# Performance work log

Hardware: AMD Instinct MI355X
Metric: run time of the kernel (lower is better)

Reference implementation:

```python
import jax, jax.numpy as jnp
import numpy as np

B, S, E = 2, 2048, 2048
H, HD = 32, 64          # n_heads, head_dim
KV, REP = 8, 4          # n_kv_head, n_kv_head_rep (H == KV*REP)
NEG = -1e9


def setup_inputs() -> dict:
    key = jax.random.key(0)
    ks = jax.random.split(key, 6)
    x = jax.random.normal(ks[0], (B, S, E), dtype=jnp.float32)
    # Llama RoPE tables: angles[p, i] = p / 10000^(2i/HD)
    inv_freq = 1.0 / (10000.0 ** (jnp.arange(0, HD, 2, dtype=jnp.float32) / HD))
    angles = jnp.arange(S, dtype=jnp.float32)[:, None] * inv_freq[None, :]  # [S, HD/2]
    cos, sin = jnp.cos(angles), jnp.sin(angles)
    # causal additive mask [S, S]
    mask = jnp.where(jnp.tril(jnp.ones((S, S), dtype=bool)), 0.0, NEG).astype(jnp.float32)
    sc = 0.02
    wq = jax.random.normal(ks[1], (E, H * HD), dtype=jnp.float32) * sc
    wk = jax.random.normal(ks[2], (E, KV * HD), dtype=jnp.float32) * sc
    wv = jax.random.normal(ks[3], (E, KV * HD), dtype=jnp.float32) * sc
    wo = jax.random.normal(ks[4], (H * HD, E), dtype=jnp.float32) * sc
    return {"x": x, "cos": cos, "sin": sin, "mask": mask,
            "wq": wq, "wk": wk, "wv": wv, "wo": wo, "start_pos": 0}


def _rope(t, cos, sin):
    # t: [B, S, h, HD]; rotate consecutive pairs (Llama complex convention)
    tp = t.reshape(t.shape[:-1] + (HD // 2, 2))
    t1, t2 = tp[..., 0], tp[..., 1]
    c = cos[None, :, None, :]
    s = sin[None, :, None, :]
    out = jnp.stack([t1 * c - t2 * s, t1 * s + t2 * c], axis=-1)
    return out.reshape(t.shape)


def reference(x, cos, sin, mask, wq, wk, wv, wo, start_pos):
    b, s, _ = x.shape
    q = (x @ wq).reshape(b, s, H, HD)
    k = (x @ wk).reshape(b, s, KV, HD)
    v = (x @ wv).reshape(b, s, KV, HD)
    q = _rope(q, cos, sin)
    k = _rope(k, cos, sin)
    # KV-cache: with start_pos=0 and full-seq prefill, the cache slice
    # [:, :start_pos+s] is exactly the freshly written k/v, so use them directly.
    # Grouped attention without materializing repeated K/V:
    # q -> [b, KV, REP, s, HD]; k,v -> [b, KV, s, HD]
    qg = q.transpose(0, 2, 1, 3).reshape(b, KV, REP, s, HD)
    kg = k.transpose(0, 2, 1, 3)
    vg = v.transpose(0, 2, 1, 3)
    scale = 1.0 / jnp.sqrt(jnp.float32(HD))
    scores = jnp.einsum('bgrqd,bgkd->bgrqk', qg, kg) * scale + mask
    attn = jax.nn.softmax(scores, axis=-1)
    og = jnp.einsum('bgrqk,bgkd->bgrqd', attn, vg)     # [b, KV, REP, s, HD]
    out = og.reshape(b, H, s, HD).transpose(0, 2, 1, 3).reshape(b, s, H * HD)
    return out @ wo
```

## Files before the change

### kernel.cpp

```cpp
#include <hip/hip_runtime.h>
#include <stdint.h>

#define S_LEN 2048
#define NTOK  4096
#define EMB   2048
#define NHEAD 32
#define HDIM  64
#define NKVH  8

typedef __bf16 bf16x8 __attribute__((ext_vector_type(8)));
typedef float  f32x4  __attribute__((ext_vector_type(4)));

#define AS1 __attribute__((address_space(1)))
#define AS3 __attribute__((address_space(3)))

#if __has_builtin(__builtin_amdgcn_exp2f)
#define EXP2(x) __builtin_amdgcn_exp2f(x)
#else
#define EXP2(x) exp2f(x)
#endif

#define QSCALE 0.1803368867f

__device__ __forceinline__ uint16_t f2bf(float f) {
  uint32_t u = __float_as_uint(f);
  u += 0x7fffu + ((u >> 16) & 1u);
  return (uint16_t)(u >> 16);
}
__device__ __forceinline__ float bf2f(uint16_t h) {
  return __uint_as_float(((uint32_t)h) << 16);
}
__device__ __forceinline__ void gld16(const void* g, void* l) {
  __builtin_amdgcn_global_load_lds((const AS1 uint32_t*)g, (AS3 uint32_t*)l, 16, 0, 0);
}
__device__ __forceinline__ f32x4 mfma16(bf16x8 a, bf16x8 b, f32x4 c) {
  return __builtin_amdgcn_mfma_f32_16x16x32_bf16(a, b, c, 0, 0, 0);
}

__global__ void k_cvt(const float* __restrict__ in, uint16_t* __restrict__ out) {
  int i = (blockIdx.x * 256 + threadIdx.x) * 4;
  float4 v = *(const float4*)(in + i);
  ushort4 o;
  o.x = f2bf(v.x); o.y = f2bf(v.y); o.z = f2bf(v.z); o.w = f2bf(v.w);
  *(ushort4*)(out + i) = o;
}

__global__ void k_transpose(const float* __restrict__ in, uint16_t* __restrict__ out,
                            int R, int C) {
  __shared__ float tile[32][33];
  int c0 = blockIdx.x * 32, r0 = blockIdx.y * 32;
  int tx = threadIdx.x & 31, ty = threadIdx.x >> 5;
#pragma unroll
  for (int j = 0; j < 32; j += 8)
    tile[ty + j][tx] = in[(size_t)(r0 + ty + j) * C + c0 + tx];
  __syncthreads();
#pragma unroll
  for (int j = 0; j < 32; j += 8)
    out[(size_t)(c0 + ty + j) * R + r0 + tx] = f2bf(tile[tx][ty + j]);
}

__global__ void k_transpose_v(const uint16_t* __restrict__ qkv, uint16_t* __restrict__ out) {
  __shared__ uint16_t tile[32][33];
  int s0 = blockIdx.x * 32, hd0 = blockIdx.y * 32, bh = blockIdx.z;
  int b = bh >> 3, kvh = bh & 7;
  int tx = threadIdx.x & 31, ty = threadIdx.x >> 5;
#pragma unroll
  for (int j = 0; j < 32; j += 8)
    tile[ty + j][tx] =
        qkv[((size_t)b * S_LEN + s0 + ty + j) * 3072 + 2560 + kvh * 64 + hd0 + tx];
  __syncthreads();
#pragma unroll
  for (int j = 0; j < 32; j += 8)
    out[((size_t)bh * 64 + hd0 + ty + j) * S_LEN + s0 + tx] = tile[tx][ty + j];
}

template <int N_REP, typename OUT_T>
__global__ __launch_bounds__(512, 1) void k_gemm256(
    const uint16_t* __restrict__ A, const uint16_t* __restrict__ BT,
    OUT_T* __restrict__ C, int M, int N, int K) {
  constexpr int ROUNDS = 4 + N_REP;
  __shared__ uint16_t lds[2][16384 + N_REP * 4096];
  const int tid = threadIdx.x, lane = tid & 63, w = tid >> 6;
  const int wm = w >> 2, wn = w & 3;
  const int l16 = lane & 15, lg = lane >> 4;
  const int nbn = N / (N_REP * 64);
  const int nwg = gridDim.x, cpx = nwg >> 3;
  const int swz = ((int)blockIdx.x & 7) * cpx + ((int)blockIdx.x >> 3);
  const int bm = (swz / nbn) * 256, bn = (swz % nbn) * (N_REP * 64);

  f32x4 acc[8][N_REP] = {};

  const int srow = tid >> 3, sslot = tid & 7;
  const int schunk = (sslot ^ (srow & 7)) * 8;
  const uint16_t* Ag = A + (size_t)(bm + srow) * K + schunk;
  const uint16_t* Bg = BT + (size_t)(bn + srow) * K + schunk;

  auto stage = [&](int d, int r, int k0) {
    if (r < 4) gld16(Ag + (size_t)r * 64 * K + k0, &lds[d][r * 4096 + tid * 8]);
    else       gld16(Bg + (size_t)(r - 4) * 64 * K + k0, &lds[d][16384 + (r - 4) * 4096 + tid * 8]);
  };
  auto lda = [&](int d, int mf, int s) -> bf16x8 {
    int row = wm * 128 + mf * 16 + l16;
    int slot = (s * 4 + lg) ^ (row & 7);
    return *(const bf16x8*)(&lds[d][row * 64 + slot * 8]);
  };
  auto ldb = [&](int d, int nf, int s) -> bf16x8 {
    int row = wn * (N_REP * 16) + nf * 16 + l16;
    int slot = (s * 4 + lg) ^ (row & 7);
    return *(const bf16x8*)(&lds[d][16384 + row * 64 + slot * 8]);
  };

  const int NT = K >> 6;
#pragma unroll
  for (int r = 0; r < ROUNDS; ++r) stage(0, r, 0);
#pragma unroll
  for (int r = 0; r < 4; ++r) if (1 < NT) stage(1, r, 64);
  asm volatile("s_waitcnt vmcnt(4)" ::: "memory");
  __builtin_amdgcn_s_barrier();

  for (int kt = 0; kt < NT; ++kt) {
    const int cur = kt & 1;
    const int nk0 = (kt + 1) << 6, nnk0 = (kt + 2) << 6;
    const bool m1 = (kt + 1 < NT), m2 = (kt + 2 < NT);
    bf16x8 a[4][2], b0[N_REP / 2][2], b1[N_REP / 2][2];
#pragma unroll
    for (int mi = 0; mi < 4; ++mi) { a[mi][0] = lda(cur, mi, 0); a[mi][1] = lda(cur, mi, 1); }
#pragma unroll
    for (int ni = 0; ni < N_REP / 2; ++ni) { b0[ni][0] = ldb(cur, ni, 0); b0[ni][1] = ldb(cur, ni, 1); }
    __builtin_amdgcn_s_barrier();
    asm volatile("s_waitcnt lgkmcnt(0)" ::: "memory");
    __builtin_amdgcn_sched_barrier(0);
    __builtin_amdgcn_s_setprio(1);
#pragma unroll
    for (int mi = 0; mi < 4; ++mi)
#pragma unroll
      for (int ni = 0; ni < N_REP / 2; ++ni) {
        acc[mi][ni] = mfma16(a[mi][0], b0[ni][0], acc[mi][ni]);
        acc[mi][ni] = mfma16(a[mi][1], b0[ni][1], acc[mi][ni]);
      }
    __builtin_amdgcn_s_setprio(0);
    __builtin_amdgcn_s_barrier();
#pragma unroll
    for (int ni = 0; ni < N_REP / 2; ++ni) { b1[ni][0] = ldb(cur, N_REP / 2 + ni, 0); b1[ni][1] = ldb(cur, N_REP / 2 + ni, 1); }
    if (m1) {
#pragma unroll
      for (int r = 4; r < 4 + N_REP / 2; ++r) stage(cur ^ 1, r, nk0);
    }
    __builtin_amdgcn_s_barrier();
    asm volatile("s_waitcnt lgkmcnt(0)" ::: "memory");
    __builtin_amdgcn_sched_barrier(0);
    __builtin_amdgcn_s_setprio(1);
#pragma unroll
    for (int mi = 0; mi < 4; ++mi)
#pragma unroll
      for (int ni = 0; ni < N_REP / 2; ++ni) {
        acc[mi][N_REP / 2 + ni] = mfma16(a[mi][0], b1[ni][0], acc[mi][N_REP / 2 + ni]);
        acc[mi][N_REP / 2 + ni] = mfma16(a[mi][1], b1[ni][1], acc[mi][N_REP / 2 + ni]);
      }
    __builtin_amdgcn_s_setprio(0);
    __builtin_amdgcn_s_barrier();
#pragma unroll
    for (int mi = 0; mi < 4; ++mi) { a[mi][0] = lda(cur, 4 + mi, 0); a[mi][1] = lda(cur, 4 + mi, 1); }
    if (m1) {
#pragma unroll
      for (int r = 4 + N_REP / 2; r < ROUNDS; ++r) stage(cur ^ 1, r, nk0);
    }
    __builtin_amdgcn_s_barrier();
    asm volatile("s_waitcnt lgkmcnt(0)" ::: "memory");
    __builtin_amdgcn_sched_barrier(0);
    __builtin_amdgcn_s_setprio(1);
#pragma unroll
    for (int mi = 0; mi < 4; ++mi)
#pragma unroll
      for (int ni = 0; ni < N_REP / 2; ++ni) {
        acc[4 + mi][N_REP / 2 + ni] = mfma16(a[mi][0], b1[ni][0], acc[4 + mi][N_REP / 2 + ni]);
        acc[4 + mi][N_REP / 2 + ni] = mfma16(a[mi][1], b1[ni][1], acc[4 + mi][N_REP / 2 + ni]);
      }
    __builtin_amdgcn_s_setprio(0);
    __builtin_amdgcn_s_barrier();
    if (m2) {
#pragma unroll
      for (int r = 0; r < 4; ++r) stage(cur, r, nnk0);
    }
    __builtin_amdgcn_s_setprio(1);
#pragma unroll
    for (int mi = 0; mi < 4; ++mi)
#pragma unroll
      for (int ni = 0; ni < N_REP / 2; ++ni) {
        acc[4 + mi][ni] = mfma16(a[mi][0], b0[ni][0], acc[4 + mi][ni]);
        acc[4 + mi][ni] = mfma16(a[mi][1], b0[ni][1], acc[4 + mi][ni]);
      }
    __builtin_amdgcn_s_setprio(0);
    if (m2) { asm volatile("s_waitcnt vmcnt(4)" ::: "memory"); }
    else    { asm volatile("s_waitcnt vmcnt(0)" ::: "memory"); }
    __builtin_amdgcn_s_barrier();
  }
#pragma unroll
  for (int mf = 0; mf < 8; ++mf)
#pragma unroll
    for (int nf = 0; nf < N_REP; ++nf)
#pragma unroll
      for (int r = 0; r < 4; ++r) {
        int row = bm + wm * 128 + mf * 16 + lg * 4 + r;
        int col = bn + wn * (N_REP * 16) + nf * 16 + l16;
        float v = acc[mf][nf][r];
        if constexpr (sizeof(OUT_T) == 4) C[(size_t)row * N + col] = v;
        else                              C[(size_t)row * N + col] = f2bf(v);
      }
}

__global__ void k_rope(const uint16_t* __restrict__ qkv, const float* __restrict__ cosT,
                       const float* __restrict__ sinT, uint16_t* __restrict__ qb,
                       uint16_t* __restrict__ kb) {
  int idx = blockIdx.x * 256 + threadIdx.x;
  int row = idx / 1280;
  int col = (idx - row * 1280) * 2;
  int s = row & (S_LEN - 1);
  uint32_t vv = *(const uint32_t*)(qkv + (size_t)row * 3072 + col);
  float t1 = bf2f((uint16_t)vv), t2 = bf2f((uint16_t)(vv >> 16));
  int i = (col & 63) >> 1;
  if (col < 2048) {
    float c = cosT[s * 32 + i] * QSCALE, sn = sinT[s * 32 + i] * QSCALE;
    uint32_t o = (uint32_t)f2bf(t1 * c - t2 * sn) | ((uint32_t)f2bf(t1 * sn + t2 * c) << 16);
    *(uint32_t*)(qb + (size_t)row * 2048 + col) = o;
  } else {
    int cc = col - 2048;
    float c = cosT[s * 32 + i], sn = sinT[s * 32 + i];
    uint32_t o = (uint32_t)f2bf(t1 * c - t2 * sn) | ((uint32_t)f2bf(t1 * sn + t2 * c) << 16);
    *(uint32_t*)(kb + (size_t)row * 512 + cc) = o;
  }
}

template <bool MASKED>
__device__ __forceinline__ void tile_compute(
    const uint16_t* Kc, const uint16_t* Vc, const bf16x8 qf[2][2], bf16x8 onesv,
    int l16, int lg, int kv0, int qb0,
    float m_r[2], f32x4 lacc[2], f32x4 acc[2][4]) {
  f32x4 st[2][4] = {};
  __builtin_amdgcn_s_setprio(1);
#pragma unroll
  for (int c = 0; c < 4; ++c) {
    int row = c * 16 + l16, sw = row & 7;
    bf16x8 ka  = *(const bf16x8*)(Kc + row * 64 + ((lg ^ sw) * 8));
    bf16x8 kb2 = *(const bf16x8*)(Kc + row * 64 + (((4 | lg) ^ sw) * 8));
#pragma unroll
    for (int qc = 0; qc < 2; ++qc) {
      st[qc][c] = mfma16(ka,  qf[qc][0], st[qc][c]);
      st[qc][c] = mfma16(kb2, qf[qc][1], st[qc][c]);
    }
  }
  __builtin_amdgcn_s_setprio(0);
  bf16x8 pu[2][2];
#pragma unroll
  for (int qc = 0; qc < 2; ++qc) {
    const int qrow = qb0 + qc * 16 + l16;
    float sv[4][4];
#pragma unroll
    for (int c = 0; c < 4; ++c)
#pragma unroll
      for (int r = 0; r < 4; ++r) {
        float s = st[qc][c][r];
        if (MASKED && (kv0 + c * 16 + lg * 4 + r > qrow)) s = -1e30f;
        sv[c][r] = s;
      }
    float m0 = fmaxf(fmaxf(sv[0][0], sv[0][1]), fmaxf(sv[0][2], sv[0][3]));
    float m1 = fmaxf(fmaxf(sv[1][0], sv[1][1]), fmaxf(sv[1][2], sv[1][3]));
    float m2 = fmaxf(fmaxf(sv[2][0], sv[2][1]), fmaxf(sv[2][2], sv[2][3]));
    float m3 = fmaxf(fmaxf(sv[3][0], sv[3][1]), fmaxf(sv[3][2], sv[3][3]));
    float mx = fmaxf(fmaxf(m0, m1), fmaxf(m2, m3));
    mx = fmaxf(mx, __shfl_xor(mx, 16));
    mx = fmaxf(mx, __shfl_xor(mx, 32));
    if (!__all(mx - m_r[qc] <= 8.0f)) {
      float m_new = fmaxf(m_r[qc], mx);
      float alpha = EXP2(m_r[qc] - m_new);
      float al[4];
#pragma unroll
      for (int r = 0; r < 4; ++r) al[r] = __shfl(alpha, lg * 4 + r);
#pragma unroll
      for (int n = 0; n < 4; ++n)
#pragma unroll
        for (int r = 0; r < 4; ++r) acc[qc][n][r] *= al[r];
#pragma unroll
      for (int r = 0; r < 4; ++r) lacc[qc][r] *= al[r];
      m_r[qc] = m_new;
    }
    float pf[4][4];
#pragma unroll
    for (int c = 0; c < 4; ++c)
#pragma unroll
      for (int r = 0; r < 4; ++r)
        pf[c][r] = EXP2(sv[c][r] - m_r[qc]);
#pragma unroll
    for (int cc = 0; cc < 2; ++cc)
#pragma unroll
      for (int e = 0; e < 8; ++e)
        ((__bf16*)&pu[qc][cc])[e] = (__bf16)pf[cc * 2 + (e >> 2)][e & 3];
  }
  __builtin_amdgcn_s_setprio(1);
#pragma unroll
  for (int cc = 0; cc < 2; ++cc) {
    lacc[0] = mfma16(pu[0][cc], onesv, lacc[0]);
    lacc[1] = mfma16(pu[1][cc], onesv, lacc[1]);
#pragma unroll
    for (int n = 0; n < 4; ++n) {
      int row = n * 16 + l16, sw2 = row & 7;
      int k0 = cc * 32 + lg * 4, k1 = k0 + 16;
      const char* base = (const char*)Vc + row * 128;
      union { uint64_t q[2]; bf16x8 v; } vu;
      vu.q[0] = *(const uint64_t*)(base + (((k0 >> 3) ^ sw2) << 4) + ((k0 & 7) << 1));
      vu.q[1] = *(const uint64_t*)(base + (((k1 >> 3) ^ sw2) << 4) + ((k1 & 7) << 1));
      acc[0][n] = mfma16(pu[0][cc], vu.v, acc[0][n]);
      acc[1][n] = mfma16(pu[1][cc], vu.v, acc[1][n]);
    }
  }
  __builtin_amdgcn_s_setprio(0);
}

__global__ __launch_bounds__(256, 3) void k_flash(
    const uint16_t* __restrict__ Qb, const uint16_t* __restrict__ Kb,
    const uint16_t* __restrict__ VT, uint16_t* __restrict__ Ob) {
  __shared__ uint16_t Ks[3][4096];
  __shared__ uint16_t Vs[3][4096];
  const int j = 63 - ((int)blockIdx.x >> 4);
  const int gb = blockIdx.x & 15;
  const int g = gb & 7, b = gb >> 3;
  const int tid = threadIdx.x, lane = tid & 63, w = tid >> 6;
  const int l16 = lane & 15, lg = lane >> 4;
  const int h = g * 4 + w;
  const int qb0 = j * 32;

  bf16x8 qf[2][2];
#pragma unroll
  for (int qc = 0; qc < 2; ++qc) {
    const size_t tokq = (size_t)b * S_LEN + qb0 + qc * 16 + l16;
    qf[qc][0] = *(const bf16x8*)(Qb + tokq * 2048 + h * 64 + lg * 8);
    qf[qc][1] = *(const bf16x8*)(Qb + tokq * 2048 + h * 64 + 32 + lg * 8);
  }
  bf16x8 onesv;
#pragma unroll
  for (int e = 0; e < 8; ++e) ((__bf16*)&onesv)[e] = (__bf16)1.0f;

  const int srow = tid >> 3, shc = tid & 7;
  const int swz = (shc ^ (srow & 7)) * 8;
  const uint16_t* Kg = Kb + ((size_t)b * S_LEN + srow) * 512 + g * 64 + swz;
  const uint16_t* Vg = VT + ((size_t)(b * 8 + g) * 64 + srow) * S_LEN + swz;

  float m_r[2] = {-1e30f, -1e30f};
  f32x4 lacc[2] = {};
  f32x4 acc[2][4] = {};
  const int nt = (j >> 1) + 1;

  auto stage = [&](int t, int buf) {
    const size_t kv0 = (size_t)t * 64;
    uint16_t* kd = &Ks[buf][tid * 8];
    uint16_t* vd = &Vs[buf][tid * 8];
    gld16(Kg + kv0 * 512, kd);
    gld16(Kg + (kv0 + 32) * 512, kd + 2048);
    gld16(Vg + kv0, vd);
    gld16(Vg + kv0 + (size_t)32 * S_LEN, vd + 2048);
  };

  stage(0, 0);
  stage(nt > 1 ? 1 : 0, 1);

  int cur = 0;
  for (int t = 0; t < nt; ++t) {
    asm volatile("s_waitcnt vmcnt(4)" ::: "memory");
    __builtin_amdgcn_s_barrier();
    {
      int ts = t + 2 < nt ? t + 2 : nt - 1;
      int bufn = cur + 2; if (bufn >= 3) bufn -= 3;
      stage(ts, bufn);
    }
    if (t == nt - 1)
      tile_compute<true >(Ks[cur], Vs[cur], qf, onesv, l16, lg, t * 64, qb0, m_r, lacc, acc);
    else
      tile_compute<false>(Ks[cur], Vs[cur], qf, onesv, l16, lg, t * 64, qb0, m_r, lacc, acc);
    cur = cur + 1 < 3 ? cur + 1 : 0;
  }
#pragma unroll
  for (int qc = 0; qc < 2; ++qc) {
    float li[4];
#pragma unroll
    for (int r = 0; r < 4; ++r) li[r] = 1.0f / lacc[qc][r];
#pragma unroll
    for (int n = 0; n < 4; ++n)
#pragma unroll
      for (int r = 0; r < 4; ++r) {
        int qo = qb0 + qc * 16 + lg * 4 + r;
        Ob[((size_t)b * S_LEN + qo) * 2048 + h * 64 + n * 16 + l16] =
            f2bf(acc[qc][n][r] * li[r]);
      }
  }
}

extern "C" void kernel_launch(void* const* d_in, const int* in_sizes, int n_in,
                              void* d_out, int out_size, void* d_ws, size_t ws_size,
                              hipStream_t stream) {
  const float* x    = (const float*)d_in[0];
  const float* cosT = (const float*)d_in[1];
  const float* sinT = (const float*)d_in[2];
  const float* wq   = (const float*)d_in[4];
  const float* wk   = (const float*)d_in[5];
  const float* wv   = (const float*)d_in[6];
  const float* wo   = (const float*)d_in[7];
  float* out = (float*)d_out;

  char* ws = (char*)d_ws;
  size_t off = 0;
  auto alloc = [&](size_t bytes) {
    void* p = ws + off;
    off += (bytes + 255) & ~(size_t)255;
    return p;
  };
  uint16_t* xb   = (uint16_t*)alloc((size_t)NTOK * EMB * 2);
  uint16_t* wT   = (uint16_t*)alloc((size_t)3072 * 2048 * 2);
  uint16_t* woT  = (uint16_t*)alloc((size_t)2048 * 2048 * 2);
  uint16_t* qkvb = (uint16_t*)alloc((size_t)NTOK * 3072 * 2);
  uint16_t* qb   = (uint16_t*)alloc((size_t)NTOK * 2048 * 2);
  uint16_t* kb   = (uint16_t*)alloc((size_t)NTOK * 512 * 2);
  uint16_t* vT   = (uint16_t*)alloc((size_t)NTOK * 512 * 2);
  uint16_t* ob   = xb;

  k_cvt<<<(NTOK * EMB) / 1024, 256, 0, stream>>>(x, xb);
  k_transpose<<<dim3(64, 64), 256, 0, stream>>>(wq, wT, 2048, 2048);
  k_transpose<<<dim3(16, 64), 256, 0, stream>>>(wk, wT + (size_t)2048 * 2048, 2048, 512);
  k_transpose<<<dim3(16, 64), 256, 0, stream>>>(wv, wT + (size_t)2560 * 2048, 2048, 512);
  k_transpose<<<dim3(64, 64), 256, 0, stream>>>(wo, woT, 2048, 2048);

  k_gemm256<4, uint16_t><<<192, 512, 0, stream>>>(xb, wT, qkvb, 4096, 3072, 2048);
  k_rope<<<(NTOK * 1280) / 256, 256, 0, stream>>>(qkvb, cosT, sinT, qb, kb);
  k_transpose_v<<<dim3(64, 2, 16), 256, 0, stream>>>(qkvb, vT);
  k_flash<<<dim3(1024), 256, 0, stream>>>(qb, kb, vT, ob);
  k_gemm256<2, float><<<256, 512, 0, stream>>>(ob, woT, out, 4096, 2048, 2048);
}
```

Before: 192.0 us.

## Use 256x192 tiles for QKV GEMM to fill all CUs, restage pipeline

Switches the QKV projection GEMM from 256x256 tiles (192 workgroups) to 256x192 tiles (N_REP=3, 256 workgroups) so every CU gets a workgroup. It also rewrites the GEMM main loop to support an odd number of B sub-tiles. All B fragments and the next B tile are loaded at the start of each iteration, and the MFMA phases are regrouped across three barrier-separated stages. This raises CU utilization for the QKV GEMM but lowers reuse per tile. It also changes the load/compute interleaving for the output GEMM, which could shift its latency hiding.

```diff
diff --git a/kernel.cpp b/kernel.cpp
--- a/kernel.cpp
+++ b/kernel.cpp
@@ -78,8 +78,8 @@
 __global__ __launch_bounds__(512, 1) void k_gemm256(
     const uint16_t* __restrict__ A, const uint16_t* __restrict__ BT,
     OUT_T* __restrict__ C, int M, int N, int K) {
-  constexpr int ROUNDS = 4 + N_REP;
-  __shared__ uint16_t lds[2][16384 + N_REP * 4096];
+  constexpr int LDSH = 16384 + N_REP * 4096;
+  __shared__ uint16_t lds[2][LDSH];
   const int tid = threadIdx.x, lane = tid & 63, w = tid >> 6;
   const int wm = w >> 2, wn = w & 3;
   const int l16 = lane & 15, lg = lane >> 4;
@@ -95,9 +95,11 @@
   const uint16_t* Ag = A + (size_t)(bm + srow) * K + schunk;
   const uint16_t* Bg = BT + (size_t)(bn + srow) * K + schunk;
 
-  auto stage = [&](int d, int r, int k0) {
-    if (r < 4) gld16(Ag + (size_t)r * 64 * K + k0, &lds[d][r * 4096 + tid * 8]);
-    else       gld16(Bg + (size_t)(r - 4) * 64 * K + k0, &lds[d][16384 + (r - 4) * 4096 + tid * 8]);
+  auto stageA = [&](int d, int r, int k0) {
+    gld16(Ag + (size_t)r * 64 * K + k0, &lds[d][r * 4096 + tid * 8]);
+  };
+  auto stageB = [&](int d, int r, int k0) {
+    gld16(Bg + (size_t)r * 64 * K + k0, &lds[d][16384 + r * 4096 + tid * 8]);
   };
   auto lda = [&](int d, int mf, int s) -> bf16x8 {
     int row = wm * 128 + mf * 16 + l16;
@@ -112,9 +114,11 @@
 
   const int NT = K >> 6;
 #pragma unroll
-  for (int r = 0; r < ROUNDS; ++r) stage(0, r, 0);
-#pragma unroll
-  for (int r = 0; r < 4; ++r) if (1 < NT) stage(1, r, 64);
+  for (int r = 0; r < 4; ++r) stageA(0, r, 0);
+#pragma unroll
+  for (int r = 0; r < N_REP; ++r) stageB(0, r, 0);
+#pragma unroll
+  for (int r = 0; r < 4; ++r) if (1 < NT) stageA(1, r, 64);
   asm volatile("s_waitcnt vmcnt(4)" ::: "memory");
   __builtin_amdgcn_s_barrier();
 
@@ -122,11 +126,15 @@
     const int cur = kt & 1;
     const int nk0 = (kt + 1) << 6, nnk0 = (kt + 2) << 6;
     const bool m1 = (kt + 1 < NT), m2 = (kt + 2 < NT);
-    bf16x8 a[4][2], b0[N_REP / 2][2], b1[N_REP / 2][2];
+    bf16x8 a[4][2], a2[4][2], b[N_REP][2];
 #pragma unroll
     for (int mi = 0; mi < 4; ++mi) { a[mi][0] = lda(cur, mi, 0); a[mi][1] = lda(cur, mi, 1); }
 #pragma unroll
-    for (int ni = 0; ni < N_REP / 2; ++ni) { b0[ni][0] = ldb(cur, ni, 0); b0[ni][1] = ldb(cur, ni, 1); }
+    for (int ni = 0; ni < N_REP; ++ni) { b[ni][0] = ldb(cur, ni, 0); b[ni][1] = ldb(cur, ni, 1); }
+    if (m1) {
+#pragma unroll
+      for (int r = 0; r < N_REP; ++r) stageB(cur ^ 1, r, nk0);
+    }
     __builtin_amdgcn_s_barrier();
     asm volatile("s_waitcnt lgkmcnt(0)" ::: "memory");
     __builtin_amdgcn_sched_barrier(0);
@@ -134,61 +142,43 @@
 #pragma unroll
     for (int mi = 0; mi < 4; ++mi)
 #pragma unroll
-      for (int ni = 0; ni < N_REP / 2; ++ni) {
-        acc[mi][ni] = mfma16(a[mi][0], b0[ni][0], acc[mi][ni]);
-        acc[mi][ni] = mfma16(a[mi][1], b0[ni][1], acc[mi][ni]);
+      for (int ni = 0; ni < 2; ++ni) {
+        acc[mi][ni] = mfma16(a[mi][0], b[ni][0], acc[mi][ni]);
+        acc[mi][ni] = mfma16(a[mi][1], b[ni][1], acc[mi][ni]);
       }
     __builtin_amdgcn_s_setprio(0);
     __builtin_amdgcn_s_barrier();
 #pragma unroll
-    for (int ni = 0; ni < N_REP / 2; ++ni) { b1[ni][0] = ldb(cur, N_REP / 2 + ni, 0); b1[ni][1] = ldb(cur, N_REP / 2 + ni, 1); }
-    if (m1) {
-#pragma unroll
-      for (int r = 4; r < 4 + N_REP / 2; ++r) stage(cur ^ 1, r, nk0);
-    }
+    for (int mi = 0; mi < 4; ++mi) { a2[mi][0] = lda(cur, 4 + mi, 0); a2[mi][1] = lda(cur, 4 + mi, 1); }
     __builtin_amdgcn_s_barrier();
     asm volatile("s_waitcnt lgkmcnt(0)" ::: "memory");
     __builtin_amdgcn_sched_barrier(0);
     __builtin_amdgcn_s_setprio(1);
+    if constexpr (N_REP == 3) {
+#pragma unroll
+      for (int mi = 0; mi < 4; ++mi) {
+        acc[mi][2] = mfma16(a[mi][0], b[2][0], acc[mi][2]);
+        acc[mi][2] = mfma16(a[mi][1], b[2][1], acc[mi][2]);
+      }
+    }
+#pragma unroll
+    for (int mi = 0; mi < 4; ++mi) {
+      acc[4 + mi][0] = mfma16(a2[mi][0], b[0][0], acc[4 + mi][0]);
+      acc[4 + mi][0] = mfma16(a2[mi][1], b[0][1], acc[4 + mi][0]);
+    }
+    __builtin_amdgcn_s_setprio(0);
+    __builtin_amdgcn_s_barrier();
+    if (m2) {
+#pragma unroll
+      for (int r = 0; r < 4; ++r) stageA(cur, r, nnk0);
+    }
+    __builtin_amdgcn_s_setprio(1);
 #pragma unroll
     for (int mi = 0; mi < 4; ++mi)
 #pragma unroll
-      for (int ni = 0; ni < N_REP / 2; ++ni) {
-        acc[mi][N_REP / 2 + ni] = mfma16(a[mi][0], b1[ni][0], acc[mi][N_REP / 2 + ni]);
-        acc[mi][N_REP / 2 + ni] = mfma16(a[mi][1], b1[ni][1], acc[mi][N_REP / 2 + ni]);
-      }
-    __builtin_amdgcn_s_setprio(0);
-    __builtin_amdgcn_s_barrier();
-#pragma unroll
-    for (int mi = 0; mi < 4; ++mi) { a[mi][0] = lda(cur, 4 + mi, 0); a[mi][1] = lda(cur, 4 + mi, 1); }
-    if (m1) {
-#pragma unroll
-      for (int r = 4 + N_REP / 2; r < ROUNDS; ++r) stage(cur ^ 1, r, nk0);
-    }
-    __builtin_amdgcn_s_barrier();
-    asm volatile("s_waitcnt lgkmcnt(0)" ::: "memory");
-    __builtin_amdgcn_sched_barrier(0);
-    __builtin_amdgcn_s_setprio(1);
-#pragma unroll
-    for (int mi = 0; mi < 4; ++mi)
-#pragma unroll
-      for (int ni = 0; ni < N_REP / 2; ++ni) {
-        acc[4 + mi][N_REP / 2 + ni] = mfma16(a[mi][0], b1[ni][0], acc[4 + mi][N_REP / 2 + ni]);
-        acc[4 + mi][N_REP / 2 + ni] = mfma16(a[mi][1], b1[ni][1], acc[4 + mi][N_REP / 2 + ni]);
-      }
-    __builtin_amdgcn_s_setprio(0);
-    __builtin_amdgcn_s_barrier();
-    if (m2) {
-#pragma unroll
-      for (int r = 0; r < 4; ++r) stage(cur, r, nnk0);
-    }
-    __builtin_amdgcn_s_setprio(1);
-#pragma unroll
-    for (int mi = 0; mi < 4; ++mi)
-#pragma unroll
-      for (int ni = 0; ni < N_REP / 2; ++ni) {
-        acc[4 + mi][ni] = mfma16(a[mi][0], b0[ni][0], acc[4 + mi][ni]);
-        acc[4 + mi][ni] = mfma16(a[mi][1], b0[ni][1], acc[4 + mi][ni]);
+      for (int ni = 1; ni < N_REP; ++ni) {
+        acc[4 + mi][ni] = mfma16(a2[mi][0], b[ni][0], acc[4 + mi][ni]);
+        acc[4 + mi][ni] = mfma16(a2[mi][1], b[ni][1], acc[4 + mi][ni]);
       }
     __builtin_amdgcn_s_setprio(0);
     if (m2) { asm volatile("s_waitcnt vmcnt(4)" ::: "memory"); }
@@ -428,7 +418,7 @@
   k_transpose<<<dim3(16, 64), 256, 0, stream>>>(wv, wT + (size_t)2560 * 2048, 2048, 512);
   k_transpose<<<dim3(64, 64), 256, 0, stream>>>(wo, woT, 2048, 2048);
 
-  k_gemm256<4, uint16_t><<<192, 512, 0, stream>>>(xb, wT, qkvb, 4096, 3072, 2048);
+  k_gemm256<3, uint16_t><<<256, 512, 0, stream>>>(xb, wT, qkvb, 4096, 3072, 2048);
   k_rope<<<(NTOK * 1280) / 256, 256, 0, stream>>>(qkvb, cosT, sinT, qb, kb);
   k_transpose_v<<<dim3(64, 2, 16), 256, 0, stream>>>(qkvb, vT);
   k_flash<<<dim3(1024), 256, 0, stream>>>(qb, kb, vT, ob);
```

New measurement: 182.5 us. 4.9% less time.
